# Kernel optimization log

Measured on AMD Instinct MI355X. Metric: run time of the kernel, lower is better.

The kernel has to match this reference:

```python
import jax, jax.numpy as jnp
import numpy as np
import math

B, LQ, LK = 2, 2048, 2048
DIM = 1024
H = 16
DH = DIM // H


def setup_inputs() -> dict:
    key = jax.random.key(0)
    ks = jax.random.split(key, 12)
    s = 1.0 / math.sqrt(DIM)
    return {
        "query": jax.random.normal(ks[0], (B, LQ, DIM), jnp.float32),
        "key": jax.random.normal(ks[1], (B, LK, DIM), jnp.float32),
        "value": jax.random.normal(ks[2], (B, LK, DIM), jnp.float32),
        "mask": jnp.zeros((B, LQ, LK), dtype=bool),
        "Wq": jax.random.normal(ks[3], (DIM, DIM), jnp.float32) * s,
        "bq": jax.random.normal(ks[4], (DIM,), jnp.float32) * s,
        "Wk": jax.random.normal(ks[5], (DIM, DIM), jnp.float32) * s,
        "bk": jax.random.normal(ks[6], (DIM,), jnp.float32) * s,
        "Wv": jax.random.normal(ks[7], (DIM, DIM), jnp.float32) * s,
        "bv": jax.random.normal(ks[8], (DIM,), jnp.float32) * s,
        "Wo": jax.random.normal(ks[9], (DIM, DIM), jnp.float32) * s,
        "bo": jax.random.normal(ks[10], (DIM,), jnp.float32) * s,
    }


def reference(query, key, value, mask, Wq, bq, Wk, bk, Wv, bv, Wo, bo):
    b = query.shape[0]

    def shape(x):  # (b, l, dim) -> (b, h, l, dh)
        return x.reshape(b, -1, H, DH).transpose(0, 2, 1, 3)

    q = shape(query @ Wq.T + bq)
    k = shape(key @ Wk.T + bk)
    v = shape(value @ Wv.T + bv)

    q = q / math.sqrt(DH)
    # (b, h, lq, lk) score matrix, computed in float32 as the original does
    scores = jnp.einsum("bhqd,bhkd->bhqk", q, k).astype(jnp.float32)
    scores = jnp.where(mask[:, None, :, :], jnp.float32(-1e18), scores)
    attn = jax.nn.softmax(scores, axis=-1).astype(q.dtype)
    context = jnp.einsum("bhqk,bhkd->bhqd", attn, v)
    context = context.transpose(0, 2, 1, 3).reshape(b, -1, H * DH)
    return context @ Wo.T + bo
```

## Files before the change

kernel.cpp:

```cpp
#include <hip/hip_runtime.h>
#include <hip/hip_bf16.h>

typedef __attribute__((ext_vector_type(4))) float float4v;
typedef __attribute__((ext_vector_type(8))) __bf16 bf16x8;
typedef __attribute__((ext_vector_type(4))) unsigned short ushort4v;

#define MFMA16(a, b, c) __builtin_amdgcn_mfma_f32_16x16x32_bf16(a, b, c, 0, 0, 0)

__device__ __forceinline__ unsigned short f2bf(float f) {
    return __builtin_bit_cast(unsigned short, (__bf16)f);
}

__device__ __forceinline__ float fast_exp2(float x) {
#if __has_builtin(__builtin_amdgcn_exp2f)
    return __builtin_amdgcn_exp2f(x);
#else
    return exp2f(x);
#endif
}

__device__ __forceinline__ void gl_lds16(const unsigned short* g, unsigned short* l) {
    __builtin_amdgcn_global_load_lds(
        (const __attribute__((address_space(1))) void*)g,
        (__attribute__((address_space(3))) void*)l, 16, 0, 0);
}

struct CvtSeg { const float* s; unsigned short* d; int n; };
struct Cvt7 { CvtSeg seg[7]; };

__global__ __launch_bounds__(256) void cvt_kernel(Cvt7 a) {
    const CvtSeg c = a.seg[blockIdx.y];
    const int stride = gridDim.x * 256 * 4;
    for (int i = (blockIdx.x * 256 + threadIdx.x) * 4; i < c.n; i += stride) {
        float4v v = *(const float4v*)(c.s + i);
        ushort4v u;
        u.x = f2bf(v.x); u.y = f2bf(v.y); u.z = f2bf(v.z); u.w = f2bf(v.w);
        *(ushort4v*)(c.d + i) = u;
    }
}

__device__ __forceinline__ void gemm128_body(const unsigned short* __restrict__ A,
                                             const unsigned short* __restrict__ W,
                                             const float* __restrict__ bias,
                                             unsigned short* __restrict__ Cout,
                                             int N, int K, float scale,
                                             unsigned short* As, unsigned short* Ws) {
    const int t = threadIdx.x;
    const int w = t >> 6, lane = t & 63;
    const int quad = lane >> 4, l16 = lane & 15;
    const int m0 = blockIdx.x * 128, n0 = blockIdx.y * 128;
    const int wm = (w >> 1) * 64, wn = (w & 1) * 64;

    float4v acc[4][4];
    for (int i = 0; i < 4; ++i)
        for (int j = 0; j < 4; ++j) acc[i][j] = float4v{0.f, 0.f, 0.f, 0.f};

    const int srow = lane >> 3;
    const int scol = (lane & 7) * 8;

    for (int k0 = 0; k0 < K; k0 += 64) {
        __syncthreads();
        for (int i = 0; i < 4; ++i) {
            const int c = w * 4 + i;
            gl_lds16(A + (size_t)(m0 + c * 8 + srow) * K + k0 + scol,
                     &As[c * 512 + lane * 8]);
            gl_lds16(W + (size_t)(n0 + c * 8 + srow) * K + k0 + scol,
                     &Ws[c * 512 + lane * 8]);
        }
        __syncthreads();
        for (int ks = 0; ks < 2; ++ks) {
            bf16x8 af[4], wf[4];
            for (int i = 0; i < 4; ++i)
                af[i] = *(const bf16x8*)&As[(wm + i * 16 + l16) * 64 + ks * 32 + quad * 8];
            for (int i = 0; i < 4; ++i)
                wf[i] = *(const bf16x8*)&Ws[(wn + i * 16 + l16) * 64 + ks * 32 + quad * 8];
            for (int mi = 0; mi < 4; ++mi)
                for (int ni = 0; ni < 4; ++ni)
                    acc[mi][ni] = MFMA16(af[mi], wf[ni], acc[mi][ni]);
        }
    }

    for (int mi = 0; mi < 4; ++mi)
        for (int ni = 0; ni < 4; ++ni) {
            const int col = n0 + wn + ni * 16 + l16;
            const float bv = bias[col];
            for (int reg = 0; reg < 4; ++reg) {
                const int row = m0 + wm + mi * 16 + quad * 4 + reg;
                Cout[(size_t)row * N + col] = f2bf((acc[mi][ni][reg] + bv) * scale);
            }
        }
}

__global__ __launch_bounds__(256) void gemm_qkv_kernel(
    const unsigned short* qa, const unsigned short* ka, const unsigned short* va,
    const unsigned short* Wqb, const unsigned short* Wkb, const unsigned short* Wvb,
    const float* bq, const float* bk, const float* bv,
    unsigned short* Qb, unsigned short* Kb, unsigned short* Vb, float qscale) {
    __shared__ unsigned short As[128 * 64];
    __shared__ unsigned short Ws[128 * 64];
    const int z = blockIdx.z;
    const unsigned short* A = z == 0 ? qa : (z == 1 ? ka : va);
    const unsigned short* W = z == 0 ? Wqb : (z == 1 ? Wkb : Wvb);
    const float* bias = z == 0 ? bq : (z == 1 ? bk : bv);
    unsigned short* C = z == 0 ? Qb : (z == 1 ? Kb : Vb);
    gemm128_body(A, W, bias, C, 1024, 1024, z == 0 ? qscale : 1.0f, As, Ws);
}

__global__ __launch_bounds__(256) void gemm_out_kernel(const unsigned short* __restrict__ A,
                                                       const unsigned short* __restrict__ W,
                                                       const float* __restrict__ bias,
                                                       float* __restrict__ Cout) {
    __shared__ unsigned short As[64 * 64];
    __shared__ unsigned short Ws[128 * 64];
    const int N = 1024, K = 1024;
    const int t = threadIdx.x;
    const int w = t >> 6, lane = t & 63;
    const int quad = lane >> 4, l16 = lane & 15;
    const int m0 = blockIdx.x * 64, n0 = blockIdx.y * 128;
    const int wm = (w & 1) * 32, wn = (w >> 1) * 64;

    float4v acc[2][4];
    for (int i = 0; i < 2; ++i)
        for (int j = 0; j < 4; ++j) acc[i][j] = float4v{0.f, 0.f, 0.f, 0.f};

    const int srow = lane >> 3;
    const int scol = (lane & 7) * 8;

    for (int k0 = 0; k0 < K; k0 += 64) {
        __syncthreads();
        for (int i = 0; i < 2; ++i) {
            const int c = w * 2 + i;
            gl_lds16(A + (size_t)(m0 + c * 8 + srow) * K + k0 + scol,
                     &As[c * 512 + lane * 8]);
        }
        for (int i = 0; i < 4; ++i) {
            const int c = w * 4 + i;
            gl_lds16(W + (size_t)(n0 + c * 8 + srow) * K + k0 + scol,
                     &Ws[c * 512 + lane * 8]);
        }
        __syncthreads();
        for (int ks = 0; ks < 2; ++ks) {
            bf16x8 af[2], wf[4];
            for (int i = 0; i < 2; ++i)
                af[i] = *(const bf16x8*)&As[(wm + i * 16 + l16) * 64 + ks * 32 + quad * 8];
            for (int i = 0; i < 4; ++i)
                wf[i] = *(const bf16x8*)&Ws[(wn + i * 16 + l16) * 64 + ks * 32 + quad * 8];
            for (int mi = 0; mi < 2; ++mi)
                for (int ni = 0; ni < 4; ++ni)
                    acc[mi][ni] = MFMA16(af[mi], wf[ni], acc[mi][ni]);
        }
    }

    for (int mi = 0; mi < 2; ++mi)
        for (int ni = 0; ni < 4; ++ni) {
            const int col = n0 + wn + ni * 16 + l16;
            const float bv = bias[col];
            for (int reg = 0; reg < 4; ++reg) {
                const int row = m0 + wm + mi * 16 + quad * 4 + reg;
                Cout[(size_t)row * N + col] = acc[mi][ni][reg] + bv;
            }
        }
}

__global__ __launch_bounds__(256) void attn_kernel(const unsigned short* __restrict__ Q,
                                                   const unsigned short* __restrict__ Kg,
                                                   const unsigned short* __restrict__ Vg,
                                                   const unsigned char* __restrict__ mask,
                                                   unsigned short* __restrict__ Ctx) {
    const int bid = blockIdx.x;
    const int qt = bid >> 5;
    const int bh = bid & 31;
    const int b = bh >> 4, h = bh & 15;
    const int t = threadIdx.x, w = t >> 6, lane = t & 63;
    const int quad = lane >> 4, l16 = lane & 15;

    __shared__ unsigned short Ps[128][72];
    __shared__ unsigned short Ks[64][72];
    __shared__ unsigned short Vt[80][72];

    const unsigned short* Qp = Q + ((size_t)(b * 2048 + qt * 128)) * 1024 + h * 64;
    const unsigned short* Kp = Kg + ((size_t)b * 2048) * 1024 + h * 64;
    const unsigned short* Vp = Vg + ((size_t)b * 2048) * 1024 + h * 64;
    const unsigned char* Mp = mask + (size_t)(b * 2048 + qt * 128) * 2048;

    for (int idx = t; idx < 16 * 72; idx += 256) {
        const int r = idx / 72, c = idx - r * 72;
        Vt[64 + r][c] = (r == 0) ? (unsigned short)0x3F80 : (unsigned short)0;
    }
    for (int p = 0; p < 4; ++p) {
        const int idx = t + p * 256;
        const int r = idx >> 3, c8 = (idx & 7) * 8;
        *(uint4*)&Ps[r][c8] = *(const uint4*)(Qp + (size_t)r * 1024 + c8);
    }
    __syncthreads();
    bf16x8 qf[2][2];
    for (int c = 0; c < 2; ++c)
        for (int ks = 0; ks < 2; ++ks)
            qf[c][ks] = *(const bf16x8*)&Ps[w * 32 + c * 16 + l16][ks * 32 + quad * 8];

    float4v o[2][5];
    for (int c = 0; c < 2; ++c)
        for (int i = 0; i < 5; ++i) o[c][i] = float4v{0.f, 0.f, 0.f, 0.f};

    const int sr = t >> 3, sc8 = (t & 7) * 8;
    const int vkk = (t & 31) * 2, vd0 = (t >> 5) * 8;
    const int mrow = w * 32 + (lane >> 1);
    const int mc0 = (lane & 1) * 32;

    uint4 kreg0, kreg1, vreg0, vreg1, mreg0, mreg1;
    {
        kreg0 = *(const uint4*)(Kp + (size_t)sr * 1024 + sc8);
        kreg1 = *(const uint4*)(Kp + (size_t)(sr + 32) * 1024 + sc8);
        vreg0 = *(const uint4*)(Vp + (size_t)vkk * 1024 + vd0);
        vreg1 = *(const uint4*)(Vp + (size_t)(vkk + 1) * 1024 + vd0);
        mreg0 = *(const uint4*)(Mp + (size_t)mrow * 2048 + mc0);
        mreg1 = *(const uint4*)(Mp + (size_t)mrow * 2048 + mc0 + 16);
    }

    for (int kc = 0; kc < 2048; kc += 64) {
        __syncthreads();
        *(uint4*)&Ks[sr][sc8] = kreg0;
        *(uint4*)&Ks[sr + 32][sc8] = kreg1;
        {
            const unsigned short* pa = (const unsigned short*)&vreg0;
            const unsigned short* pb = (const unsigned short*)&vreg1;
            for (int j = 0; j < 8; ++j)
                *(unsigned int*)&Vt[vd0 + j][vkk] =
                    (unsigned int)pa[j] | ((unsigned int)pb[j] << 16);
        }
        const unsigned int mor = mreg0.x | mreg0.y | mreg0.z | mreg0.w |
                                 mreg1.x | mreg1.y | mreg1.z | mreg1.w;
        const bool anymask = __any(mor != 0);
        __syncthreads();

        const int kn = kc + 64;
        if (kn < 2048) {
            kreg0 = *(const uint4*)(Kp + (size_t)(kn + sr) * 1024 + sc8);
            kreg1 = *(const uint4*)(Kp + (size_t)(kn + sr + 32) * 1024 + sc8);
            vreg0 = *(const uint4*)(Vp + (size_t)(kn + vkk) * 1024 + vd0);
            vreg1 = *(const uint4*)(Vp + (size_t)(kn + vkk + 1) * 1024 + vd0);
            mreg0 = *(const uint4*)(Mp + (size_t)mrow * 2048 + kn + mc0);
            mreg1 = *(const uint4*)(Mp + (size_t)mrow * 2048 + kn + mc0 + 16);
        }

        float4v s0[4], s1[4];
        for (int nt = 0; nt < 4; ++nt) {
            const float4v z4 = float4v{0.f, 0.f, 0.f, 0.f};
            bf16x8 kf = *(const bf16x8*)&Ks[nt * 16 + l16][quad * 8];
            s0[nt] = MFMA16(qf[0][0], kf, z4);
            s1[nt] = MFMA16(qf[1][0], kf, z4);
            kf = *(const bf16x8*)&Ks[nt * 16 + l16][32 + quad * 8];
            s0[nt] = MFMA16(qf[0][1], kf, s0[nt]);
            s1[nt] = MFMA16(qf[1][1], kf, s1[nt]);
        }

        for (int c = 0; c < 2; ++c) {
            float4v* s = c ? s1 : s0;
            for (int reg = 0; reg < 4; ++reg) {
                float sv[4];
                for (int nt = 0; nt < 4; ++nt) sv[nt] = s[nt][reg];
                if (anymask) {
                    const unsigned char* mr =
                        Mp + (size_t)(w * 32 + c * 16 + quad * 4 + reg) * 2048 + kc;
                    for (int nt = 0; nt < 4; ++nt)
                        if (mr[nt * 16 + l16]) sv[nt] = -1e18f;
                }
                for (int nt = 0; nt < 4; ++nt)
                    Ps[w * 32 + c * 16 + quad * 4 + reg][nt * 16 + l16] =
                        f2bf(fast_exp2(sv[nt]));
            }
        }

        bf16x8 pf0[2], pf1[2];
        for (int ks = 0; ks < 2; ++ks) {
            pf0[ks] = *(const bf16x8*)&Ps[w * 32 + l16][ks * 32 + quad * 8];
            pf1[ks] = *(const bf16x8*)&Ps[w * 32 + 16 + l16][ks * 32 + quad * 8];
        }
        for (int ks = 0; ks < 2; ++ks)
            for (int dt = 0; dt < 5; ++dt) {
                bf16x8 vf = *(const bf16x8*)&Vt[dt * 16 + l16][ks * 32 + quad * 8];
                o[0][dt] = MFMA16(pf0[ks], vf, o[0][dt]);
                o[1][dt] = MFMA16(pf1[ks], vf, o[1][dt]);
            }
    }

    for (int c = 0; c < 2; ++c) {
        float inv[4];
        for (int reg = 0; reg < 4; ++reg)
            inv[reg] = 1.0f / __shfl(o[c][4][reg], lane & 48);
        for (int dt = 0; dt < 4; ++dt) {
            const int dcol = dt * 16 + l16;
            for (int reg = 0; reg < 4; ++reg) {
                const int ql = w * 32 + c * 16 + quad * 4 + reg;
                Ctx[((size_t)(b * 2048 + qt * 128 + ql)) * 1024 + h * 64 + dcol] =
                    f2bf(o[c][dt][reg] * inv[reg]);
            }
        }
    }
}

extern "C" void kernel_launch(void* const* d_in, const int* in_sizes, int n_in,
                              void* d_out, int out_size, void* d_ws, size_t ws_size,
                              hipStream_t stream) {
    (void)in_sizes; (void)n_in; (void)out_size; (void)ws_size;
    const float* query = (const float*)d_in[0];
    const float* key   = (const float*)d_in[1];
    const float* value = (const float*)d_in[2];
    const unsigned char* mask = (const unsigned char*)d_in[3];
    const float* Wq = (const float*)d_in[4];
    const float* bq = (const float*)d_in[5];
    const float* Wk = (const float*)d_in[6];
    const float* bk = (const float*)d_in[7];
    const float* Wv = (const float*)d_in[8];
    const float* bv = (const float*)d_in[9];
    const float* Wo = (const float*)d_in[10];
    const float* bo = (const float*)d_in[11];

    const size_t MD = (size_t)4096 * 1024;
    const size_t WD = (size_t)1024 * 1024;

    unsigned short* Qb  = (unsigned short*)d_ws;
    unsigned short* Kb  = Qb + MD;
    unsigned short* Vb  = Kb + MD;
    unsigned short* qb  = Vb + MD;
    unsigned short* kb  = qb + MD;
    unsigned short* vb  = kb + MD;
    unsigned short* Wqb = vb + MD;
    unsigned short* Wkb = Wqb + WD;
    unsigned short* Wvb = Wkb + WD;
    unsigned short* Wob = Wvb + WD;
    unsigned short* Cb  = qb;

    Cvt7 cv;
    cv.seg[0] = {query, qb, (int)MD};
    cv.seg[1] = {key,   kb, (int)MD};
    cv.seg[2] = {value, vb, (int)MD};
    cv.seg[3] = {Wq, Wqb, (int)WD};
    cv.seg[4] = {Wk, Wkb, (int)WD};
    cv.seg[5] = {Wv, Wvb, (int)WD};
    cv.seg[6] = {Wo, Wob, (int)WD};
    cvt_kernel<<<dim3(1024, 7), 256, 0, stream>>>(cv);

    const float qscale = 0.125f * 1.44269504088896f;
    gemm_qkv_kernel<<<dim3(32, 8, 3), 256, 0, stream>>>(
        qb, kb, vb, Wqb, Wkb, Wvb, bq, bk, bv, Qb, Kb, Vb, qscale);

    attn_kernel<<<dim3(512), 256, 0, stream>>>(Qb, Kb, Vb, mask, Cb);

    gemm_out_kernel<<<dim3(64, 8), 256, 0, stream>>>(Cb, Wob, bo, (float*)d_out);
}
```

Before: 278.6 us.

## Split attention over two key halves and merge partials in a combine kernel

```diff
diff --git a/kernel.cpp b/kernel.cpp
--- a/kernel.cpp
+++ b/kernel.cpp
@@ -166,10 +166,12 @@
                                                    const unsigned short* __restrict__ Kg,
                                                    const unsigned short* __restrict__ Vg,
                                                    const unsigned char* __restrict__ mask,
-                                                   unsigned short* __restrict__ Ctx) {
+                                                   float* __restrict__ Op,
+                                                   float* __restrict__ Lp) {
     const int bid = blockIdx.x;
-    const int qt = bid >> 5;
     const int bh = bid & 31;
+    const int sp = (bid >> 5) & 1;
+    const int qt = bid >> 6;
     const int b = bh >> 4, h = bh & 15;
     const int t = threadIdx.x, w = t >> 6, lane = t & 63;
     const int quad = lane >> 4, l16 = lane & 15;
@@ -178,10 +180,11 @@
     __shared__ unsigned short Ks[64][72];
     __shared__ unsigned short Vt[80][72];
 
+    const int kbase = sp * 1024;
     const unsigned short* Qp = Q + ((size_t)(b * 2048 + qt * 128)) * 1024 + h * 64;
-    const unsigned short* Kp = Kg + ((size_t)b * 2048) * 1024 + h * 64;
-    const unsigned short* Vp = Vg + ((size_t)b * 2048) * 1024 + h * 64;
-    const unsigned char* Mp = mask + (size_t)(b * 2048 + qt * 128) * 2048;
+    const unsigned short* Kp = Kg + ((size_t)(b * 2048 + kbase)) * 1024 + h * 64;
+    const unsigned short* Vp = Vg + ((size_t)(b * 2048 + kbase)) * 1024 + h * 64;
+    const unsigned char* Mp = mask + (size_t)(b * 2048 + qt * 128) * 2048 + kbase;
 
     for (int idx = t; idx < 16 * 72; idx += 256) {
         const int r = idx / 72, c = idx - r * 72;
@@ -217,7 +220,7 @@
         mreg1 = *(const uint4*)(Mp + (size_t)mrow * 2048 + mc0 + 16);
     }
 
-    for (int kc = 0; kc < 2048; kc += 64) {
+    for (int kc = 0; kc < 1024; kc += 64) {
         __syncthreads();
         *(uint4*)&Ks[sr][sc8] = kreg0;
         *(uint4*)&Ks[sr + 32][sc8] = kreg1;
@@ -234,7 +237,7 @@
         __syncthreads();
 
         const int kn = kc + 64;
-        if (kn < 2048) {
+        if (kn < 1024) {
             kreg0 = *(const uint4*)(Kp + (size_t)(kn + sr) * 1024 + sc8);
             kreg1 = *(const uint4*)(Kp + (size_t)(kn + sr + 32) * 1024 + sc8);
             vreg0 = *(const uint4*)(Vp + (size_t)(kn + vkk) * 1024 + vd0);
@@ -284,19 +287,40 @@
             }
     }
 
+    float* Opp = Op + (size_t)sp * 4096 * 1024;
+    float* Lpp = Lp + (size_t)sp * 65536;
     for (int c = 0; c < 2; ++c) {
-        float inv[4];
-        for (int reg = 0; reg < 4; ++reg)
-            inv[reg] = 1.0f / __shfl(o[c][4][reg], lane & 48);
+        for (int reg = 0; reg < 4; ++reg) {
+            const int ql = w * 32 + c * 16 + quad * 4 + reg;
+            const int grow = b * 2048 + qt * 128 + ql;
+            if (l16 == 0) Lpp[(size_t)grow * 16 + h] = o[c][4][reg];
+        }
         for (int dt = 0; dt < 4; ++dt) {
             const int dcol = dt * 16 + l16;
             for (int reg = 0; reg < 4; ++reg) {
                 const int ql = w * 32 + c * 16 + quad * 4 + reg;
-                Ctx[((size_t)(b * 2048 + qt * 128 + ql)) * 1024 + h * 64 + dcol] =
-                    f2bf(o[c][dt][reg] * inv[reg]);
-            }
-        }
-    }
+                const int grow = b * 2048 + qt * 128 + ql;
+                Opp[(size_t)grow * 1024 + h * 64 + dcol] = o[c][dt][reg];
+            }
+        }
+    }
+}
+
+__global__ __launch_bounds__(256) void combine_kernel(const float* __restrict__ Op,
+                                                      const float* __restrict__ Lp,
+                                                      unsigned short* __restrict__ Cb) {
+    const size_t e = ((size_t)blockIdx.x * 256 + threadIdx.x) * 4;
+    const int row = (int)(e >> 10);
+    const int h = ((int)e & 1023) >> 6;
+    float4v a = *(const float4v*)(Op + e);
+    float4v bq = *(const float4v*)(Op + (size_t)4096 * 1024 + e);
+    const float inv = 1.0f / (Lp[(size_t)row * 16 + h] + Lp[65536 + (size_t)row * 16 + h]);
+    ushort4v u;
+    u.x = f2bf((a.x + bq.x) * inv);
+    u.y = f2bf((a.y + bq.y) * inv);
+    u.z = f2bf((a.z + bq.z) * inv);
+    u.w = f2bf((a.w + bq.w) * inv);
+    *(ushort4v*)(Cb + e) = u;
 }
 
 extern "C" void kernel_launch(void* const* d_in, const int* in_sizes, int n_in,
@@ -328,8 +352,10 @@
     unsigned short* Wqb = vb + MD;
     unsigned short* Wkb = Wqb + WD;
     unsigned short* Wvb = Wkb + WD;
-    unsigned short* Wob = Wvb + WD;
-    unsigned short* Cb  = qb;
+    float* Op = (float*)qb;
+    unsigned short* Wob = qb + 4 * MD;
+    unsigned short* Cb  = Wob + WD;
+    float* Lp = (float*)(Cb + MD);
 
     Cvt7 cv;
     cv.seg[0] = {query, qb, (int)MD};
@@ -345,7 +371,9 @@
     gemm_qkv_kernel<<<dim3(32, 8, 3), 256, 0, stream>>>(
         qb, kb, vb, Wqb, Wkb, Wvb, bq, bk, bv, Qb, Kb, Vb, qscale);
 
-    attn_kernel<<<dim3(512), 256, 0, stream>>>(Qb, Kb, Vb, mask, Cb);
+    attn_kernel<<<dim3(1024), 256, 0, stream>>>(Qb, Kb, Vb, mask, Op, Lp);
+
+    combine_kernel<<<dim3(4096), 256, 0, stream>>>(Op, Lp, Cb);
 
     gemm_out_kernel<<<dim3(64, 8), 256, 0, stream>>>(Cb, Wob, bo, (float*)d_out);
 }
```

Result: no change. 276.2 us (-0.9%).

## Halve attention query tile to 64 rows and accumulate row sums in registers

Applied to the files above, without the earlier changes.

```diff
diff --git a/kernel.cpp b/kernel.cpp
--- a/kernel.cpp
+++ b/kernel.cpp
@@ -168,53 +168,47 @@
                                                    const unsigned char* __restrict__ mask,
                                                    unsigned short* __restrict__ Ctx) {
     const int bid = blockIdx.x;
+    const int bh = bid & 31;
     const int qt = bid >> 5;
-    const int bh = bid & 31;
     const int b = bh >> 4, h = bh & 15;
     const int t = threadIdx.x, w = t >> 6, lane = t & 63;
     const int quad = lane >> 4, l16 = lane & 15;
 
-    __shared__ unsigned short Ps[128][72];
+    __shared__ unsigned short Pt[64][72];
     __shared__ unsigned short Ks[64][72];
-    __shared__ unsigned short Vt[80][72];
-
-    const unsigned short* Qp = Q + ((size_t)(b * 2048 + qt * 128)) * 1024 + h * 64;
+    __shared__ unsigned short Vt[64][72];
+
+    const unsigned short* Qp = Q + ((size_t)(b * 2048 + qt * 64)) * 1024 + h * 64;
     const unsigned short* Kp = Kg + ((size_t)b * 2048) * 1024 + h * 64;
     const unsigned short* Vp = Vg + ((size_t)b * 2048) * 1024 + h * 64;
-    const unsigned char* Mp = mask + (size_t)(b * 2048 + qt * 128) * 2048;
-
-    for (int idx = t; idx < 16 * 72; idx += 256) {
-        const int r = idx / 72, c = idx - r * 72;
-        Vt[64 + r][c] = (r == 0) ? (unsigned short)0x3F80 : (unsigned short)0;
-    }
-    for (int p = 0; p < 4; ++p) {
-        const int idx = t + p * 256;
-        const int r = idx >> 3, c8 = (idx & 7) * 8;
-        *(uint4*)&Ps[r][c8] = *(const uint4*)(Qp + (size_t)r * 1024 + c8);
+    const unsigned char* Mp = mask + (size_t)(b * 2048 + qt * 64) * 2048;
+
+    {
+        const int r = t >> 3, c8 = (t & 7) * 8;
+        *(uint4*)&Pt[r][c8] = *(const uint4*)(Qp + (size_t)r * 1024 + c8);
+        *(uint4*)&Pt[r + 32][c8] = *(const uint4*)(Qp + (size_t)(r + 32) * 1024 + c8);
     }
     __syncthreads();
-    bf16x8 qf[2][2];
-    for (int c = 0; c < 2; ++c)
-        for (int ks = 0; ks < 2; ++ks)
-            qf[c][ks] = *(const bf16x8*)&Ps[w * 32 + c * 16 + l16][ks * 32 + quad * 8];
-
-    float4v o[2][5];
-    for (int c = 0; c < 2; ++c)
-        for (int i = 0; i < 5; ++i) o[c][i] = float4v{0.f, 0.f, 0.f, 0.f};
+    bf16x8 qf[2];
+    qf[0] = *(const bf16x8*)&Pt[w * 16 + l16][quad * 8];
+    qf[1] = *(const bf16x8*)&Pt[w * 16 + l16][32 + quad * 8];
+
+    float4v o[4];
+    for (int i = 0; i < 4; ++i) o[i] = float4v{0.f, 0.f, 0.f, 0.f};
+    float l_acc = 0.f;
 
     const int sr = t >> 3, sc8 = (t & 7) * 8;
     const int vkk = (t & 31) * 2, vd0 = (t >> 5) * 8;
-    const int mrow = w * 32 + (lane >> 1);
-    const int mc0 = (lane & 1) * 32;
-
-    uint4 kreg0, kreg1, vreg0, vreg1, mreg0, mreg1;
+    const int mrow = w * 16 + (lane >> 2);
+    const int mc0 = (lane & 3) * 16;
+
+    uint4 kreg0, kreg1, vreg0, vreg1, mreg;
     {
         kreg0 = *(const uint4*)(Kp + (size_t)sr * 1024 + sc8);
         kreg1 = *(const uint4*)(Kp + (size_t)(sr + 32) * 1024 + sc8);
         vreg0 = *(const uint4*)(Vp + (size_t)vkk * 1024 + vd0);
         vreg1 = *(const uint4*)(Vp + (size_t)(vkk + 1) * 1024 + vd0);
-        mreg0 = *(const uint4*)(Mp + (size_t)mrow * 2048 + mc0);
-        mreg1 = *(const uint4*)(Mp + (size_t)mrow * 2048 + mc0 + 16);
+        mreg  = *(const uint4*)(Mp + (size_t)mrow * 2048 + mc0);
     }
 
     for (int kc = 0; kc < 2048; kc += 64) {
@@ -228,9 +222,7 @@
                 *(unsigned int*)&Vt[vd0 + j][vkk] =
                     (unsigned int)pa[j] | ((unsigned int)pb[j] << 16);
         }
-        const unsigned int mor = mreg0.x | mreg0.y | mreg0.z | mreg0.w |
-                                 mreg1.x | mreg1.y | mreg1.z | mreg1.w;
-        const bool anymask = __any(mor != 0);
+        const bool anymask = __any((mreg.x | mreg.y | mreg.z | mreg.w) != 0);
         __syncthreads();
 
         const int kn = kc + 64;
@@ -239,62 +231,59 @@
             kreg1 = *(const uint4*)(Kp + (size_t)(kn + sr + 32) * 1024 + sc8);
             vreg0 = *(const uint4*)(Vp + (size_t)(kn + vkk) * 1024 + vd0);
             vreg1 = *(const uint4*)(Vp + (size_t)(kn + vkk + 1) * 1024 + vd0);
-            mreg0 = *(const uint4*)(Mp + (size_t)mrow * 2048 + kn + mc0);
-            mreg1 = *(const uint4*)(Mp + (size_t)mrow * 2048 + kn + mc0 + 16);
-        }
-
-        float4v s0[4], s1[4];
+            mreg  = *(const uint4*)(Mp + (size_t)mrow * 2048 + kn + mc0);
+        }
+
+        float4v s[4];
         for (int nt = 0; nt < 4; ++nt) {
             const float4v z4 = float4v{0.f, 0.f, 0.f, 0.f};
             bf16x8 kf = *(const bf16x8*)&Ks[nt * 16 + l16][quad * 8];
-            s0[nt] = MFMA16(qf[0][0], kf, z4);
-            s1[nt] = MFMA16(qf[1][0], kf, z4);
+            s[nt] = MFMA16(kf, qf[0], z4);
             kf = *(const bf16x8*)&Ks[nt * 16 + l16][32 + quad * 8];
-            s0[nt] = MFMA16(qf[0][1], kf, s0[nt]);
-            s1[nt] = MFMA16(qf[1][1], kf, s1[nt]);
-        }
-
-        for (int c = 0; c < 2; ++c) {
-            float4v* s = c ? s1 : s0;
-            for (int reg = 0; reg < 4; ++reg) {
-                float sv[4];
-                for (int nt = 0; nt < 4; ++nt) sv[nt] = s[nt][reg];
-                if (anymask) {
-                    const unsigned char* mr =
-                        Mp + (size_t)(w * 32 + c * 16 + quad * 4 + reg) * 2048 + kc;
-                    for (int nt = 0; nt < 4; ++nt)
-                        if (mr[nt * 16 + l16]) sv[nt] = -1e18f;
-                }
-                for (int nt = 0; nt < 4; ++nt)
-                    Ps[w * 32 + c * 16 + quad * 4 + reg][nt * 16 + l16] =
-                        f2bf(fast_exp2(sv[nt]));
+            s[nt] = MFMA16(kf, qf[1], s[nt]);
+        }
+
+        for (int nt = 0; nt < 4; ++nt) {
+            float p0 = s[nt][0], p1 = s[nt][1], p2 = s[nt][2], p3 = s[nt][3];
+            if (anymask) {
+                const unsigned char* mr =
+                    Mp + (size_t)(w * 16 + l16) * 2048 + kc + nt * 16 + quad * 4;
+                if (mr[0]) p0 = -1e18f;
+                if (mr[1]) p1 = -1e18f;
+                if (mr[2]) p2 = -1e18f;
+                if (mr[3]) p3 = -1e18f;
             }
-        }
-
-        bf16x8 pf0[2], pf1[2];
+            const float e0 = fast_exp2(p0), e1 = fast_exp2(p1);
+            const float e2 = fast_exp2(p2), e3 = fast_exp2(p3);
+            l_acc += (e0 + e1) + (e2 + e3);
+            uint2 u;
+            u.x = (unsigned int)f2bf(e0) | ((unsigned int)f2bf(e1) << 16);
+            u.y = (unsigned int)f2bf(e2) | ((unsigned int)f2bf(e3) << 16);
+            *(uint2*)&Pt[w * 16 + l16][nt * 16 + quad * 4] = u;
+        }
+
         for (int ks = 0; ks < 2; ++ks) {
-            pf0[ks] = *(const bf16x8*)&Ps[w * 32 + l16][ks * 32 + quad * 8];
-            pf1[ks] = *(const bf16x8*)&Ps[w * 32 + 16 + l16][ks * 32 + quad * 8];
-        }
-        for (int ks = 0; ks < 2; ++ks)
-            for (int dt = 0; dt < 5; ++dt) {
+            bf16x8 pf = *(const bf16x8*)&Pt[w * 16 + l16][ks * 32 + quad * 8];
+            for (int dt = 0; dt < 4; ++dt) {
                 bf16x8 vf = *(const bf16x8*)&Vt[dt * 16 + l16][ks * 32 + quad * 8];
-                o[0][dt] = MFMA16(pf0[ks], vf, o[0][dt]);
-                o[1][dt] = MFMA16(pf1[ks], vf, o[1][dt]);
+                o[dt] = MFMA16(pf, vf, o[dt]);
             }
-    }
-
-    for (int c = 0; c < 2; ++c) {
-        float inv[4];
-        for (int reg = 0; reg < 4; ++reg)
-            inv[reg] = 1.0f / __shfl(o[c][4][reg], lane & 48);
-        for (int dt = 0; dt < 4; ++dt) {
-            const int dcol = dt * 16 + l16;
-            for (int reg = 0; reg < 4; ++reg) {
-                const int ql = w * 32 + c * 16 + quad * 4 + reg;
-                Ctx[((size_t)(b * 2048 + qt * 128 + ql)) * 1024 + h * 64 + dcol] =
-                    f2bf(o[c][dt][reg] * inv[reg]);
-            }
+        }
+    }
+
+    float lfull = l_acc;
+    lfull += __shfl_xor(lfull, 16);
+    lfull += __shfl_xor(lfull, 32);
+    float inv[4];
+    for (int reg = 0; reg < 4; ++reg)
+        inv[reg] = 1.0f / __shfl(lfull, (lane & 48) | (quad * 4 + reg));
+
+    for (int dt = 0; dt < 4; ++dt) {
+        const int dcol = dt * 16 + l16;
+        for (int reg = 0; reg < 4; ++reg) {
+            const int ql = w * 16 + quad * 4 + reg;
+            Ctx[((size_t)(b * 2048 + qt * 64 + ql)) * 1024 + h * 64 + dcol] =
+                f2bf(o[dt][reg] * inv[reg]);
         }
     }
 }
@@ -345,7 +334,7 @@
     gemm_qkv_kernel<<<dim3(32, 8, 3), 256, 0, stream>>>(
         qb, kb, vb, Wqb, Wkb, Wvb, bq, bk, bv, Qb, Kb, Vb, qscale);
 
-    attn_kernel<<<dim3(512), 256, 0, stream>>>(Qb, Kb, Vb, mask, Cb);
+    attn_kernel<<<dim3(1024), 256, 0, stream>>>(Qb, Kb, Vb, mask, Cb);
 
     gemm_out_kernel<<<dim3(64, 8), 256, 0, stream>>>(Cb, Wob, bo, (float*)d_out);
 }
```

Measured after the change: 268.6 us. 1.04x faster.
